# Optimization experiments

Hardware: AMD Instinct MI355X
Metric: run time of the kernel (lower is better)

## Reference

```python
import jax, jax.numpy as jnp
import numpy as np

N, D, E = 100000, 128, 1600000
BN_EPS = 1e-5

def setup_inputs() -> dict:
    key = jax.random.key(0)
    k1, k2, k3 = jax.random.split(key, 3)
    src_embeddings = jax.random.normal(k1, (N, D), dtype=jnp.float32)
    dst_embeddings = jax.random.normal(k2, (N, D), dtype=jnp.float32)
    graph = jax.random.randint(k3, (2, E), 0, N, dtype=jnp.int64)
    bn_weight = jnp.ones((1,), dtype=jnp.float32)
    bn_bias = jnp.zeros((1,), dtype=jnp.float32)
    return {
        "src_embeddings": src_embeddings,
        "dst_embeddings": dst_embeddings,
        "graph": graph,
        "bn_weight": bn_weight,
        "bn_bias": bn_bias,
    }

def reference(src_embeddings, dst_embeddings, graph, bn_weight, bn_bias):
    # gather endpoint embeddings by edge indices: [E, D]
    src = src_embeddings[graph[0]]
    dst = dst_embeddings[graph[1]]
    # squared distance per edge, clamped as in torch .clamp(min=1e-12)
    d2 = jnp.clip(jnp.sum((src - dst) ** 2, axis=-1), 1e-12, None)  # [E]
    likelihood = -jnp.log(d2)
    # BatchNorm1d(1) in training mode: batch mean, biased variance, eps=1e-5
    mu = jnp.mean(likelihood)
    var = jnp.mean((likelihood - mu) ** 2)
    edge_weights_logits = bn_weight[0] * (likelihood - mu) * jax.lax.rsqrt(var + BN_EPS) + bn_bias[0]
    # weighting_function = torch.sigmoid
    edge_weights = jax.nn.sigmoid(edge_weights_logits)
    # normalize=True: divide by mean
    edge_weights = edge_weights / jnp.mean(edge_weights)
    edge_weights = edge_weights[:, None]  # [E, 1]
    return graph, edge_weights, edge_weights_logits
```

## Files before the change

kernel.cpp:

```cpp
#include <hip/hip_runtime.h>
#include <math.h>

#define EMB_D 128
#define BN_EPS 1e-5f

typedef float v2f __attribute__((ext_vector_type(2)));

#if defined(__has_builtin)
#if __has_builtin(__builtin_amdgcn_cvt_pk_f32_fp8) && __has_builtin(__builtin_amdgcn_cvt_pk_fp8_f32)
#define FP8_HW 1
#endif
#endif

__device__ __forceinline__ unsigned int sw_f32_to_fp8(float x) {
    unsigned int u = __float_as_uint(x);
    unsigned int s = u >> 31;
    int e = (int)((u >> 23) & 0xff) - 127;
    unsigned int m = u & 0x7fffff;
    m += 0x7FFFF + ((m >> 20) & 1);
    if (m >> 23) { m = 0; e += 1; }
    int e8 = e + 7;
    if (e8 <= 0) return s << 7;
    if (e8 >= 15) return (s << 7) | 0x7E;
    return (s << 7) | ((unsigned)e8 << 3) | (m >> 20);
}

__device__ __forceinline__ float sw_fp8_to_f32(unsigned int v) {
    unsigned int s = (v >> 7) & 1, e = (v >> 3) & 15, m = v & 7;
    if (e == 0) return 0.0f;
    unsigned int bits = (s << 31) | ((e - 7 + 127) << 23) | (m << 20);
    return __uint_as_float(bits);
}

__device__ __forceinline__ unsigned int pack4_fp8(float4 v) {
#ifdef FP8_HW
    unsigned int o = 0;
    o = (unsigned int)__builtin_amdgcn_cvt_pk_fp8_f32(v.x, v.y, (int)o, false);
    o = (unsigned int)__builtin_amdgcn_cvt_pk_fp8_f32(v.z, v.w, (int)o, true);
    return o;
#else
    return sw_f32_to_fp8(v.x) | (sw_f32_to_fp8(v.y) << 8) |
           (sw_f32_to_fp8(v.z) << 16) | (sw_f32_to_fp8(v.w) << 24);
#endif
}

__device__ __forceinline__ float fp8x4_d2(unsigned int ua, unsigned int ub) {
#ifdef FP8_HW
    v2f a0 = __builtin_amdgcn_cvt_pk_f32_fp8((int)ua, false);
    v2f a1 = __builtin_amdgcn_cvt_pk_f32_fp8((int)ua, true);
    v2f b0 = __builtin_amdgcn_cvt_pk_f32_fp8((int)ub, false);
    v2f b1 = __builtin_amdgcn_cvt_pk_f32_fp8((int)ub, true);
    float dx = a0.x - b0.x, dy = a0.y - b0.y;
    float dz = a1.x - b1.x, dw = a1.y - b1.y;
#else
    float dx = sw_fp8_to_f32(ua & 0xff)         - sw_fp8_to_f32(ub & 0xff);
    float dy = sw_fp8_to_f32((ua >> 8) & 0xff)  - sw_fp8_to_f32((ub >> 8) & 0xff);
    float dz = sw_fp8_to_f32((ua >> 16) & 0xff) - sw_fp8_to_f32((ub >> 16) & 0xff);
    float dw = sw_fp8_to_f32(ua >> 24)          - sw_fp8_to_f32(ub >> 24);
#endif
    return fmaf(dx, dx, fmaf(dy, dy, fmaf(dz, dz, dw * dw)));
}

__device__ __forceinline__ float chunk_d2(uint4 a, uint4 b) {
    return fp8x4_d2(a.x, b.x) + fp8x4_d2(a.y, b.y)
         + fp8x4_d2(a.z, b.z) + fp8x4_d2(a.w, b.w);
}

__global__ void prep_kernel(const float* __restrict__ src,
                            const float* __restrict__ dst,
                            unsigned int* __restrict__ src8,
                            unsigned int* __restrict__ dst8,
                            long long nElem,
                            const int* __restrict__ g,
                            float* __restrict__ out_graph,
                            long long twoE,
                            double* __restrict__ acc)
{
    if (blockIdx.x == 0 && threadIdx.x < 3) acc[threadIdx.x] = 0.0;

    const long long nthreads = (long long)gridDim.x * blockDim.x;
    const long long tid0 = (long long)blockIdx.x * blockDim.x + threadIdx.x;

    const long long nvec = nElem / 4;
    for (long long i = tid0; i < nvec; i += nthreads)
        src8[i] = pack4_fp8(((const float4*)src)[i]);
    for (long long i = tid0; i < nvec; i += nthreads)
        dst8[i] = pack4_fp8(((const float4*)dst)[i]);

    const long long gvec = twoE / 4;
    for (long long i = tid0; i < gvec; i += nthreads) {
        const int4 v = ((const int4*)g)[i];
        float4 f;
        f.x = (float)v.x; f.y = (float)v.y; f.z = (float)v.z; f.w = (float)v.w;
        ((float4*)out_graph)[i] = f;
    }
    for (long long i = gvec * 4 + tid0; i < twoE; i += nthreads)
        out_graph[i] = (float)g[i];
}

__global__ void edge_l_fp8_kernel(const unsigned char* __restrict__ src8,
                                  const unsigned char* __restrict__ dst8,
                                  const int* __restrict__ g,
                                  long long E,
                                  float*  __restrict__ l_out,
                                  double* __restrict__ acc)
{
    const int sub = threadIdx.x & 1;
    const int eg  = threadIdx.x >> 1;
    const long long stride = (long long)gridDim.x * 128;

    double sumL = 0.0, sumL2 = 0.0;

    long long e = (long long)blockIdx.x * 128 + eg;
    int s = 0, d = 0;
    if (e < E) { s = g[e]; d = g[E + e]; }

    while (e < E) {
        const long long en = e + stride;
        int sn = 0, dn = 0;
        if (en < E) { sn = g[en]; dn = g[E + en]; }

        const uint4* sa = (const uint4*)(src8 + (long long)s * 128) + sub * 4;
        const uint4* sb = (const uint4*)(dst8 + (long long)d * 128) + sub * 4;
        const uint4 a0 = sa[0], a1 = sa[1], a2 = sa[2], a3 = sa[3];
        const uint4 b0 = sb[0], b1 = sb[1], b2 = sb[2], b3 = sb[3];

        float p = chunk_d2(a0, b0) + chunk_d2(a1, b1)
                + chunk_d2(a2, b2) + chunk_d2(a3, b3);

        p += __shfl_xor(p, 1, 64);

        if (sub == 0) {
            const float L = -logf(fmaxf(p, 1e-12f));
            l_out[e] = L;
            sumL  += (double)L;
            sumL2 += (double)L * (double)L;
        }
        e = en; s = sn; d = dn;
    }

    __shared__ double sA[256];
    __shared__ double sB[256];
    sA[threadIdx.x] = sumL;
    sB[threadIdx.x] = sumL2;
    __syncthreads();
    for (int ofs = 128; ofs >= 1; ofs >>= 1) {
        if ((int)threadIdx.x < ofs) {
            sA[threadIdx.x] += sA[threadIdx.x + ofs];
            sB[threadIdx.x] += sB[threadIdx.x + ofs];
        }
        __syncthreads();
    }
    if (threadIdx.x == 0) {
        atomicAdd(&acc[0], sA[0]);
        atomicAdd(&acc[1], sB[0]);
    }
}

__global__ void edge_l_kernel(const float* __restrict__ src,
                              const float* __restrict__ dst,
                              const int*   __restrict__ g,
                              long long E,
                              float*  __restrict__ l_out,
                              double* __restrict__ acc)
{
    const int sub  = threadIdx.x & 7;
    const int egrp = threadIdx.x >> 3;
    const long long stride = (long long)gridDim.x * 32;

    double sumL = 0.0, sumL2 = 0.0;

    long long e = (long long)blockIdx.x * 32 + egrp;
    int s = 0, d = 0;
    if (e < E) { s = g[e]; d = g[E + e]; }

    while (e < E) {
        const long long en = e + stride;
        int sn = 0, dn = 0;
        if (en < E) { sn = g[en]; dn = g[E + en]; }

        const float4* sa = (const float4*)(src + (long long)s * EMB_D);
        const float4* sb = (const float4*)(dst + (long long)d * EMB_D);
        const float4 a0 = sa[sub];      const float4 b0 = sb[sub];
        const float4 a1 = sa[sub + 8];  const float4 b1 = sb[sub + 8];
        const float4 a2 = sa[sub + 16]; const float4 b2 = sb[sub + 16];
        const float4 a3 = sa[sub + 24]; const float4 b3 = sb[sub + 24];

        float dx, dy, dz, dw, p = 0.f;
        dx = a0.x-b0.x; dy = a0.y-b0.y; dz = a0.z-b0.z; dw = a0.w-b0.w;
        p += fmaf(dx,dx,fmaf(dy,dy,fmaf(dz,dz,dw*dw)));
        dx = a1.x-b1.x; dy = a1.y-b1.y; dz = a1.z-b1.z; dw = a1.w-b1.w;
        p += fmaf(dx,dx,fmaf(dy,dy,fmaf(dz,dz,dw*dw)));
        dx = a2.x-b2.x; dy = a2.y-b2.y; dz = a2.z-b2.z; dw = a2.w-b2.w;
        p += fmaf(dx,dx,fmaf(dy,dy,fmaf(dz,dz,dw*dw)));
        dx = a3.x-b3.x; dy = a3.y-b3.y; dz = a3.z-b3.z; dw = a3.w-b3.w;
        p += fmaf(dx,dx,fmaf(dy,dy,fmaf(dz,dz,dw*dw)));

        p += __shfl_xor(p, 1, 64);
        p += __shfl_xor(p, 2, 64);
        p += __shfl_xor(p, 4, 64);

        if (sub == 0) {
            const float L = -logf(fmaxf(p, 1e-12f));
            l_out[e] = L;
            sumL  += (double)L;
            sumL2 += (double)L * (double)L;
        }
        e = en; s = sn; d = dn;
    }

    __shared__ double sA[256];
    __shared__ double sB[256];
    sA[threadIdx.x] = sumL;
    sB[threadIdx.x] = sumL2;
    __syncthreads();
    for (int ofs = 128; ofs >= 1; ofs >>= 1) {
        if ((int)threadIdx.x < ofs) {
            sA[threadIdx.x] += sA[threadIdx.x + ofs];
            sB[threadIdx.x] += sB[threadIdx.x + ofs];
        }
        __syncthreads();
    }
    if (threadIdx.x == 0) {
        atomicAdd(&acc[0], sA[0]);
        atomicAdd(&acc[1], sB[0]);
    }
}

__global__ void copy_graph_kernel(const int* __restrict__ g,
                                  float* __restrict__ out,
                                  long long n)
{
    const long long nthreads = (long long)gridDim.x * blockDim.x;
    const long long tid0 = (long long)blockIdx.x * blockDim.x + threadIdx.x;
    const long long nvec = n / 4;
    for (long long i = tid0; i < nvec; i += nthreads) {
        const int4 v = ((const int4*)g)[i];
        float4 f;
        f.x = (float)v.x; f.y = (float)v.y; f.z = (float)v.z; f.w = (float)v.w;
        ((float4*)out)[i] = f;
    }
    for (long long i = nvec * 4 + tid0; i < n; i += nthreads)
        out[i] = (float)g[i];
}

__global__ void bn_sig_kernel(float* __restrict__ logits,
                              float* __restrict__ ew,
                              const double* __restrict__ acc,
                              double* __restrict__ sig_acc,
                              const float* __restrict__ bn_w,
                              const float* __restrict__ bn_b,
                              long long E)
{
    const long long nthreads = (long long)gridDim.x * blockDim.x;
    const long long tid0 = (long long)blockIdx.x * blockDim.x + threadIdx.x;

    __shared__ float s_mu, s_inv, s_w, s_b;
    if (threadIdx.x == 0) {
        const double mu  = acc[0] / (double)E;
        const double var = acc[1] / (double)E - mu * mu;
        s_mu  = (float)mu;
        s_inv = (float)(1.0 / sqrt(var + (double)BN_EPS));
        s_w   = bn_w[0];
        s_b   = bn_b[0];
    }
    __syncthreads();
    const float mu = s_mu, inv = s_inv, w = s_w, b = s_b;

    double sig = 0.0;
    for (long long i = tid0; i < E; i += nthreads) {
        const float L = logits[i];
        const float z = w * (L - mu) * inv + b;
        logits[i] = z;
        const float sg = 1.0f / (1.0f + expf(-z));
        ew[i] = sg;
        sig += (double)sg;
    }

    __shared__ double sS[256];
    sS[threadIdx.x] = sig;
    __syncthreads();
    for (int ofs = 128; ofs >= 1; ofs >>= 1) {
        if ((int)threadIdx.x < ofs)
            sS[threadIdx.x] += sS[threadIdx.x + ofs];
        __syncthreads();
    }
    if (threadIdx.x == 0)
        atomicAdd(sig_acc, sS[0]);
}

__global__ void norm_kernel(float* __restrict__ ew,
                            const double* __restrict__ sig_acc,
                            long long E)
{
    const long long nthreads = (long long)gridDim.x * blockDim.x;
    const long long tid0 = (long long)blockIdx.x * blockDim.x + threadIdx.x;
    const float scale = (float)((double)E / sig_acc[0]);

    const long long nvec = E / 4;
    for (long long i = tid0; i < nvec; i += nthreads) {
        float4 v = ((float4*)ew)[i];
        v.x *= scale; v.y *= scale; v.z *= scale; v.w *= scale;
        ((float4*)ew)[i] = v;
    }
    for (long long i = nvec * 4 + tid0; i < E; i += nthreads)
        ew[i] *= scale;
}

extern "C" void kernel_launch(void* const* d_in, const int* in_sizes, int n_in,
                              void* d_out, int out_size, void* d_ws, size_t ws_size,
                              hipStream_t stream) {
    const float* src  = (const float*)d_in[0];
    const float* dst  = (const float*)d_in[1];
    const int*   g    = (const int*)d_in[2];
    const float* bn_w = (const float*)d_in[3];
    const float* bn_b = (const float*)d_in[4];

    const long long N = (long long)in_sizes[0] / EMB_D;
    const long long E = (long long)in_sizes[2] / 2;

    float* out        = (float*)d_out;
    float* out_graph  = out;
    float* out_ew     = out + 2 * E;
    float* out_logits = out + 3 * E;

    double* acc = (double*)d_ws;
    unsigned char* src8 = (unsigned char*)d_ws + 256;
    unsigned char* dst8 = src8 + (size_t)N * EMB_D;
    const size_t need = 256 + (size_t)N * EMB_D * 2;

    if (ws_size >= need) {
        prep_kernel<<<4096, 256, 0, stream>>>(src, dst,
                                              (unsigned int*)src8,
                                              (unsigned int*)dst8,
                                              N * EMB_D, g, out_graph, 2 * E, acc);
        edge_l_fp8_kernel<<<4096, 256, 0, stream>>>(src8, dst8, g, E,
                                                    out_logits, acc);
    } else {
        hipMemsetAsync(d_ws, 0, 3 * sizeof(double), stream);
        copy_graph_kernel<<<2048, 256, 0, stream>>>(g, out_graph, 2 * E);
        edge_l_kernel<<<4096, 256, 0, stream>>>(src, dst, g, E, out_logits, acc);
    }

    bn_sig_kernel<<<2048, 256, 0, stream>>>(out_logits, out_ew, acc, &acc[2],
                                            bn_w, bn_b, E);
    norm_kernel<<<2048, 256, 0, stream>>>(out_ew, &acc[2], E);
}
```

Measured before the change: 293.0 us.

## Bin edges by endpoint slices so each XCD gathers an L2-resident subset

Adds a binning pass that packs each edge's src, dst and id into a 64-bit record and groups records into 64 buckets by source and destination node slices. The gather kernel assigns eight buckets to each XCD so the fp8 embedding rows it touches can stay resident in that XCD's L2. The graph-to-float copy moves into the final normalization kernel. In exchange it adds an extra pass that writes and rereads the records, scattered logit writes, and a capped overflow region that could silently drop edges if the buckets are very skewed.

Measured after the change: 293.8 us. No clear change (+0.3%).

```diff
diff --git a/kernel.cpp b/kernel.cpp
--- a/kernel.cpp
+++ b/kernel.cpp
@@ -3,6 +3,8 @@
 
 #define EMB_D 128
 #define BN_EPS 1e-5f
+#define GATHER_BLOCKS 2048
+#define OVF_CAP 8192
 
 typedef float v2f __attribute__((ext_vector_type(2)));
 
@@ -66,77 +68,154 @@
          + fp8x4_d2(a.z, b.z) + fp8x4_d2(a.w, b.w);
 }
 
+__device__ __forceinline__ float edge_L(const unsigned char* src8,
+                                        const unsigned char* dst8,
+                                        int s, int d, int sub) {
+    const uint4* sa = (const uint4*)(src8 + (long long)s * 128) + sub * 4;
+    const uint4* sb = (const uint4*)(dst8 + (long long)d * 128) + sub * 4;
+    const uint4 a0 = sa[0], a1 = sa[1], a2 = sa[2], a3 = sa[3];
+    const uint4 b0 = sb[0], b1 = sb[1], b2 = sb[2], b3 = sb[3];
+    float p = chunk_d2(a0, b0) + chunk_d2(a1, b1)
+            + chunk_d2(a2, b2) + chunk_d2(a3, b3);
+    p += __shfl_xor(p, 1, 64);
+    return -logf(fmaxf(p, 1e-12f));
+}
+
 __global__ void prep_kernel(const float* __restrict__ src,
                             const float* __restrict__ dst,
                             unsigned int* __restrict__ src8,
                             unsigned int* __restrict__ dst8,
                             long long nElem,
-                            const int* __restrict__ g,
-                            float* __restrict__ out_graph,
-                            long long twoE,
-                            double* __restrict__ acc)
-{
-    if (blockIdx.x == 0 && threadIdx.x < 3) acc[threadIdx.x] = 0.0;
-
+                            double* __restrict__ acc,
+                            unsigned int* __restrict__ cursors,
+                            unsigned int cap)
+{
+    if (blockIdx.x == 0) {
+        if (threadIdx.x < 65) cursors[threadIdx.x] = threadIdx.x * cap;
+        if (threadIdx.x >= 65 && threadIdx.x < 68) acc[threadIdx.x - 65] = 0.0;
+    }
     const long long nthreads = (long long)gridDim.x * blockDim.x;
     const long long tid0 = (long long)blockIdx.x * blockDim.x + threadIdx.x;
-
     const long long nvec = nElem / 4;
     for (long long i = tid0; i < nvec; i += nthreads)
         src8[i] = pack4_fp8(((const float4*)src)[i]);
     for (long long i = tid0; i < nvec; i += nthreads)
         dst8[i] = pack4_fp8(((const float4*)dst)[i]);
-
-    const long long gvec = twoE / 4;
-    for (long long i = tid0; i < gvec; i += nthreads) {
-        const int4 v = ((const int4*)g)[i];
-        float4 f;
-        f.x = (float)v.x; f.y = (float)v.y; f.z = (float)v.z; f.w = (float)v.w;
-        ((float4*)out_graph)[i] = f;
-    }
-    for (long long i = gvec * 4 + tid0; i < twoE; i += nthreads)
-        out_graph[i] = (float)g[i];
-}
-
-__global__ void edge_l_fp8_kernel(const unsigned char* __restrict__ src8,
-                                  const unsigned char* __restrict__ dst8,
-                                  const int* __restrict__ g,
-                                  long long E,
-                                  float*  __restrict__ l_out,
-                                  double* __restrict__ acc)
+}
+
+__global__ void bin_kernel(const int* __restrict__ g,
+                           long long E,
+                           unsigned long long* __restrict__ rec,
+                           unsigned int* __restrict__ cursors,
+                           unsigned int cap,
+                           float inv_slice)
+{
+    __shared__ unsigned int hist[64];
+    __shared__ unsigned int curs[64];
+
+    const long long chunkSz = (long long)blockDim.x * 8;
+    const long long nchunks = (E + chunkSz - 1) / chunkSz;
+
+    for (long long c = blockIdx.x; c < nchunks; c += gridDim.x) {
+        const long long base = c * chunkSz;
+        if (threadIdx.x < 64) hist[threadIdx.x] = 0;
+        __syncthreads();
+
+        int bb[8];
+        unsigned long long pk[8];
+        #pragma unroll
+        for (int k = 0; k < 8; ++k) {
+            const long long e = base + (long long)k * blockDim.x + threadIdx.x;
+            bb[k] = -1;
+            if (e < E) {
+                const unsigned int s = (unsigned int)g[e];
+                const unsigned int d = (unsigned int)g[E + e];
+                int bs = (int)((float)s * inv_slice); bs = bs > 7 ? 7 : bs;
+                int bd = (int)((float)d * inv_slice); bd = bd > 7 ? 7 : bd;
+                bb[k] = bs * 8 + bd;
+                pk[k] = (unsigned long long)s | ((unsigned long long)d << 20)
+                      | ((unsigned long long)e << 40);
+                atomicAdd(&hist[bb[k]], 1u);
+            }
+        }
+        __syncthreads();
+        if (threadIdx.x < 64 && hist[threadIdx.x] > 0)
+            curs[threadIdx.x] = atomicAdd(&cursors[threadIdx.x], hist[threadIdx.x]);
+        __syncthreads();
+
+        #pragma unroll
+        for (int k = 0; k < 8; ++k) {
+            if (bb[k] >= 0) {
+                unsigned int off = atomicAdd(&curs[bb[k]], 1u);
+                const unsigned int lim = (unsigned int)(bb[k] + 1) * cap;
+                if (off < lim) {
+                    rec[off] = pk[k];
+                } else {
+                    unsigned int oo = atomicAdd(&cursors[64], 1u);
+                    if (oo < 64u * cap + OVF_CAP) rec[oo] = pk[k];
+                }
+            }
+        }
+        __syncthreads();
+    }
+}
+
+__global__ void edge_l_binned_kernel(const unsigned char* __restrict__ src8,
+                                     const unsigned char* __restrict__ dst8,
+                                     const unsigned long long* __restrict__ rec,
+                                     const unsigned int* __restrict__ cursors,
+                                     unsigned int cap,
+                                     float* __restrict__ l_out,
+                                     double* __restrict__ acc)
 {
     const int sub = threadIdx.x & 1;
     const int eg  = threadIdx.x >> 1;
-    const long long stride = (long long)gridDim.x * 128;
+    const int xcd = blockIdx.x & 7;
+    const int local = blockIdx.x >> 3;
+    const unsigned int perXcd = gridDim.x >> 3;
+    const unsigned int stride = perXcd * 128;
 
     double sumL = 0.0, sumL2 = 0.0;
 
-    long long e = (long long)blockIdx.x * 128 + eg;
-    int s = 0, d = 0;
-    if (e < E) { s = g[e]; d = g[E + e]; }
-
-    while (e < E) {
-        const long long en = e + stride;
-        int sn = 0, dn = 0;
-        if (en < E) { sn = g[en]; dn = g[E + en]; }
-
-        const uint4* sa = (const uint4*)(src8 + (long long)s * 128) + sub * 4;
-        const uint4* sb = (const uint4*)(dst8 + (long long)d * 128) + sub * 4;
-        const uint4 a0 = sa[0], a1 = sa[1], a2 = sa[2], a3 = sa[3];
-        const uint4 b0 = sb[0], b1 = sb[1], b2 = sb[2], b3 = sb[3];
-
-        float p = chunk_d2(a0, b0) + chunk_d2(a1, b1)
-                + chunk_d2(a2, b2) + chunk_d2(a3, b3);
-
-        p += __shfl_xor(p, 1, 64);
-
-        if (sub == 0) {
-            const float L = -logf(fmaxf(p, 1e-12f));
-            l_out[e] = L;
-            sumL  += (double)L;
-            sumL2 += (double)L * (double)L;
-        }
-        e = en; s = sn; d = dn;
+    for (int j = 0; j < 8; ++j) {
+        const int b = xcd * 8 + j;
+        const unsigned int start = (unsigned int)b * cap;
+        unsigned int end = cursors[b];
+        const unsigned int lim = (unsigned int)(b + 1) * cap;
+        if (end > lim) end = lim;
+        for (unsigned int idx = start + (unsigned int)local * 128u + eg;
+             idx < end; idx += stride) {
+            const unsigned long long v = rec[idx];
+            const int s = (int)(v & 0xFFFFFu);
+            const int d = (int)((v >> 20) & 0xFFFFFu);
+            const long long eid = (long long)(v >> 40);
+            const float L = edge_L(src8, dst8, s, d, sub);
+            if (sub == 0) {
+                l_out[eid] = L;
+                sumL  += (double)L;
+                sumL2 += (double)L * (double)L;
+            }
+        }
+    }
+
+    {
+        const unsigned int start = 64u * cap;
+        unsigned int end = cursors[64];
+        if (end > start + OVF_CAP) end = start + OVF_CAP;
+        const unsigned int gstride = gridDim.x * 128u;
+        for (unsigned int idx = start + blockIdx.x * 128u + eg;
+             idx < end; idx += gstride) {
+            const unsigned long long v = rec[idx];
+            const int s = (int)(v & 0xFFFFFu);
+            const int d = (int)((v >> 20) & 0xFFFFFu);
+            const long long eid = (long long)(v >> 40);
+            const float L = edge_L(src8, dst8, s, d, sub);
+            if (sub == 0) {
+                l_out[eid] = L;
+                sumL  += (double)L;
+                sumL2 += (double)L * (double)L;
+            }
+        }
     }
 
     __shared__ double sA[256];
@@ -157,6 +236,54 @@
     }
 }
 
+__global__ void edge_l_fp8_kernel(const unsigned char* __restrict__ src8,
+                                  const unsigned char* __restrict__ dst8,
+                                  const int* __restrict__ g,
+                                  long long E,
+                                  float*  __restrict__ l_out,
+                                  double* __restrict__ acc)
+{
+    const int sub = threadIdx.x & 1;
+    const int eg  = threadIdx.x >> 1;
+    const long long stride = (long long)gridDim.x * 128;
+
+    double sumL = 0.0, sumL2 = 0.0;
+
+    long long e = (long long)blockIdx.x * 128 + eg;
+    int s = 0, d = 0;
+    if (e < E) { s = g[e]; d = g[E + e]; }
+
+    while (e < E) {
+        const long long en = e + stride;
+        int sn = 0, dn = 0;
+        if (en < E) { sn = g[en]; dn = g[E + en]; }
+        const float L = edge_L(src8, dst8, s, d, sub);
+        if (sub == 0) {
+            l_out[e] = L;
+            sumL  += (double)L;
+            sumL2 += (double)L * (double)L;
+        }
+        e = en; s = sn; d = dn;
+    }
+
+    __shared__ double sA[256];
+    __shared__ double sB[256];
+    sA[threadIdx.x] = sumL;
+    sB[threadIdx.x] = sumL2;
+    __syncthreads();
+    for (int ofs = 128; ofs >= 1; ofs >>= 1) {
+        if ((int)threadIdx.x < ofs) {
+            sA[threadIdx.x] += sA[threadIdx.x + ofs];
+            sB[threadIdx.x] += sB[threadIdx.x + ofs];
+        }
+        __syncthreads();
+    }
+    if (threadIdx.x == 0) {
+        atomicAdd(&acc[0], sA[0]);
+        atomicAdd(&acc[1], sB[0]);
+    }
+}
+
 __global__ void edge_l_kernel(const float* __restrict__ src,
                               const float* __restrict__ dst,
                               const int*   __restrict__ g,
@@ -227,23 +354,6 @@
     }
 }
 
-__global__ void copy_graph_kernel(const int* __restrict__ g,
-                                  float* __restrict__ out,
-                                  long long n)
-{
-    const long long nthreads = (long long)gridDim.x * blockDim.x;
-    const long long tid0 = (long long)blockIdx.x * blockDim.x + threadIdx.x;
-    const long long nvec = n / 4;
-    for (long long i = tid0; i < nvec; i += nthreads) {
-        const int4 v = ((const int4*)g)[i];
-        float4 f;
-        f.x = (float)v.x; f.y = (float)v.y; f.z = (float)v.z; f.w = (float)v.w;
-        ((float4*)out)[i] = f;
-    }
-    for (long long i = nvec * 4 + tid0; i < n; i += nthreads)
-        out[i] = (float)g[i];
-}
-
 __global__ void bn_sig_kernel(float* __restrict__ logits,
                               float* __restrict__ ew,
                               const double* __restrict__ acc,
@@ -289,9 +399,11 @@
         atomicAdd(sig_acc, sS[0]);
 }
 
-__global__ void norm_kernel(float* __restrict__ ew,
-                            const double* __restrict__ sig_acc,
-                            long long E)
+__global__ void norm_graph_kernel(float* __restrict__ ew,
+                                  const double* __restrict__ sig_acc,
+                                  const int* __restrict__ g,
+                                  float* __restrict__ out_graph,
+                                  long long E)
 {
     const long long nthreads = (long long)gridDim.x * blockDim.x;
     const long long tid0 = (long long)blockIdx.x * blockDim.x + threadIdx.x;
@@ -305,6 +417,16 @@
     }
     for (long long i = nvec * 4 + tid0; i < E; i += nthreads)
         ew[i] *= scale;
+
+    const long long gvec = (2 * E) / 4;
+    for (long long i = tid0; i < gvec; i += nthreads) {
+        const int4 v = ((const int4*)g)[i];
+        float4 f;
+        f.x = (float)v.x; f.y = (float)v.y; f.z = (float)v.z; f.w = (float)v.w;
+        ((float4*)out_graph)[i] = f;
+    }
+    for (long long i = gvec * 4 + tid0; i < 2 * E; i += nthreads)
+        out_graph[i] = (float)g[i];
 }
 
 extern "C" void kernel_launch(void* const* d_in, const int* in_sizes, int n_in,
@@ -324,25 +446,41 @@
     float* out_ew     = out + 2 * E;
     float* out_logits = out + 3 * E;
 
-    double* acc = (double*)d_ws;
-    unsigned char* src8 = (unsigned char*)d_ws + 256;
-    unsigned char* dst8 = src8 + (size_t)N * EMB_D;
-    const size_t need = 256 + (size_t)N * EMB_D * 2;
-
-    if (ws_size >= need) {
+    double*       acc     = (double*)d_ws;
+    unsigned int* cursors = (unsigned int*)((char*)d_ws + 64);
+    unsigned char* src8   = (unsigned char*)d_ws + 512;
+    unsigned char* dst8   = src8 + (size_t)N * EMB_D;
+    unsigned long long* rec = (unsigned long long*)(dst8 + (size_t)N * EMB_D);
+
+    const unsigned int cap = (unsigned int)(E / 64 + 2048);
+    const size_t need_full = 512 + (size_t)N * EMB_D * 2
+                           + ((size_t)64 * cap + OVF_CAP) * 8;
+    const size_t need_fp8  = 512 + (size_t)N * EMB_D * 2;
+
+    const int slice_sz = (int)((N + 7) / 8);
+    const float inv_slice = 1.0f / (float)slice_sz;
+
+    if (ws_size >= need_full && N < (1 << 20) && E < (1LL << 24)) {
         prep_kernel<<<4096, 256, 0, stream>>>(src, dst,
                                               (unsigned int*)src8,
                                               (unsigned int*)dst8,
-                                              N * EMB_D, g, out_graph, 2 * E, acc);
+                                              N * EMB_D, acc, cursors, cap);
+        bin_kernel<<<1024, 256, 0, stream>>>(g, E, rec, cursors, cap, inv_slice);
+        edge_l_binned_kernel<<<GATHER_BLOCKS, 256, 0, stream>>>(
+            src8, dst8, rec, cursors, cap, out_logits, acc);
+    } else if (ws_size >= need_fp8) {
+        prep_kernel<<<4096, 256, 0, stream>>>(src, dst,
+                                              (unsigned int*)src8,
+                                              (unsigned int*)dst8,
+                                              N * EMB_D, acc, cursors, cap);
         edge_l_fp8_kernel<<<4096, 256, 0, stream>>>(src8, dst8, g, E,
                                                     out_logits, acc);
     } else {
         hipMemsetAsync(d_ws, 0, 3 * sizeof(double), stream);
-        copy_graph_kernel<<<2048, 256, 0, stream>>>(g, out_graph, 2 * E);
         edge_l_kernel<<<4096, 256, 0, stream>>>(src, dst, g, E, out_logits, acc);
     }
 
     bn_sig_kernel<<<2048, 256, 0, stream>>>(out_logits, out_ew, acc, &acc[2],
                                             bn_w, bn_b, E);
-    norm_kernel<<<2048, 256, 0, stream>>>(out_ew, &acc[2], E);
-}
+    norm_graph_kernel<<<2048, 256, 0, stream>>>(out_ew, &acc[2], g, out_graph, E);
+}
```
